# Kernel optimization log

Hardware: AMD Instinct MI355X
Metric: run time of the kernel (lower is better)

Reference implementation:

```python
import jax, jax.numpy as jnp
import numpy as np

DIM = 256
WS = 7          # window_size
NH = 8          # num_heads
HD = DIM // NH  # head_dim = 32
SCALE = HD ** (-0.5)
B = 4096        # batch * num_windows
N = WS * WS     # 49 tokens per window


def _rel_pos_index(ws):
    coords = np.stack(np.meshgrid(np.arange(ws), np.arange(ws), indexing='ij'))
    cf = coords.transpose(1, 2, 0).reshape(-1, 2)                 # [N,2]
    rel = cf[:, None, :] - cf[None, :, :]                          # [N,N,2]
    rel[:, :, 0] += ws - 1
    rel[:, :, 1] += ws - 1
    rel[:, :, 0] *= 2 * ws - 1
    return jnp.asarray(rel.sum(-1).astype(np.int32))               # [N,N]

REL_IDX = _rel_pos_index(WS)


def setup_inputs() -> dict:
    key = jax.random.key(0)
    ks = jax.random.split(key, 8)
    x = jax.random.normal(ks[0], (B, N, DIM), dtype=jnp.float32)
    mask = jax.random.normal(ks[1], (B, 1, N, N), dtype=jnp.float32)
    qkv_w = jax.random.normal(ks[2], (DIM, 3 * DIM), dtype=jnp.float32) * 0.02
    qkv_b = jnp.zeros((3 * DIM,), dtype=jnp.float32)
    rpb_table = jax.random.normal(ks[3], ((2 * WS - 1) ** 2, NH), dtype=jnp.float32) * 0.02
    proj_w = jax.random.normal(ks[4], (DIM, DIM), dtype=jnp.float32) * 0.02
    proj_b = jnp.zeros((DIM,), dtype=jnp.float32)
    return {"x": x, "mask": mask, "qkv_w": qkv_w, "qkv_b": qkv_b,
            "rpb_table": rpb_table, "proj_w": proj_w, "proj_b": proj_b}


def reference(x, mask, qkv_w, qkv_b, rpb_table, proj_w, proj_b):
    b, n, c = x.shape
    qkv = x @ qkv_w + qkv_b                                        # [b,n,3c]
    qkv = qkv.reshape(b, n, 3, NH, HD).transpose(2, 0, 3, 1, 4)    # [3,b,h,n,d]
    q, k, v = qkv[0], qkv[1], qkv[2]
    attn = jnp.einsum('bhnd,bhmd->bhnm', q * SCALE, k)             # [b,h,n,n]
    bias = rpb_table[REL_IDX.reshape(-1)].reshape(n, n, NH)        # [n,n,h]
    attn = attn + bias.transpose(2, 0, 1)[None] + mask             # [b,h,n,n]
    attn = jax.nn.softmax(attn, axis=-1)
    out = jnp.einsum('bhnm,bhmd->bhnd', attn, v)                   # [b,h,n,d]
    out = out.transpose(0, 2, 1, 3).reshape(b, n, c)               # [b,n,c]
    return out @ proj_w + proj_b
```

## Files before the change

### kernel.cpp

```cpp
#include <hip/hip_runtime.h>
#include <cstdint>
#include <cstddef>


#define NTOK 49
#define SCALE 0.17677669529663687f

typedef unsigned short u16;
typedef __attribute__((ext_vector_type(8))) short short8;
typedef __attribute__((ext_vector_type(4))) float f32x4;

__device__ __forceinline__ u16 f2bf(float f) {
    unsigned int u = __float_as_uint(f);
    u = (u + 0x7FFFu + ((u >> 16) & 1u)) >> 16;
    return (u16)u;
}

__device__ __forceinline__ void async_lds16(void* lds, const void* g) {
    __builtin_amdgcn_global_load_lds(
        (const __attribute__((address_space(1))) void*)g,
        (__attribute__((address_space(3))) void*)lds, 16, 0, 0);
}

__global__ void prep_weights(const float* __restrict__ qkv_w,
                             const float* __restrict__ proj_w,
                             u16* __restrict__ qkv_wT,
                             u16* __restrict__ proj_wT) {
    int i = blockIdx.x * 256 + threadIdx.x;
    if (i < 768 * 256) {
        int oc = i >> 8, k = i & 255;
        qkv_wT[i] = f2bf(qkv_w[k * 768 + oc]);
    }
    int j = i - 768 * 256;
    if (j >= 0 && j < 256 * 256) {
        int oc = j >> 8, k = j & 255;
        proj_wT[j] = f2bf(proj_w[k * 256 + oc]);
    }
}

__global__ __launch_bounds__(512, 4) void qkv_gemm(
        const float* __restrict__ x, const u16* __restrict__ wT,
        const float* __restrict__ bias, u16* __restrict__ qkv) {
    __shared__ __align__(16) u16 As[128 * 64];
    __shared__ __align__(16) u16 Bs[256 * 64];
    const int bid = blockIdx.x;
    const int m0 = (bid % 1568) * 128, n0 = (bid / 1568) * 256;
    const int t = threadIdx.x;
    const int lane = t & 63, w = t >> 6;
    const int quad = lane >> 4, l16 = lane & 15;
    const int wm = w & 1, wn = w >> 1;
    const int ar = t >> 2, ac = (t & 3) * 16;
    const int br = t >> 3, bc = (t & 7) * 8;
    f32x4 acc[4][4] = {};
    for (int kk = 0; kk < 256; kk += 64) {
        #pragma unroll
        for (int c = 0; c < 4; ++c)
            async_lds16(&Bs[c * 4096 + t * 8],
                        wT + (size_t)(n0 + c * 64 + br) * 256 + kk + bc);
        {
            const float* src = x + (size_t)(m0 + ar) * 256 + kk + ac;
            const f32x4 v0 = *(const f32x4*)(src);
            const f32x4 v1 = *(const f32x4*)(src + 4);
            const f32x4 v2 = *(const f32x4*)(src + 8);
            const f32x4 v3 = *(const f32x4*)(src + 12);
            ushort4 p0, p1, p2, p3;
            p0.x=f2bf(v0.x); p0.y=f2bf(v0.y); p0.z=f2bf(v0.z); p0.w=f2bf(v0.w);
            p1.x=f2bf(v1.x); p1.y=f2bf(v1.y); p1.z=f2bf(v1.z); p1.w=f2bf(v1.w);
            p2.x=f2bf(v2.x); p2.y=f2bf(v2.y); p2.z=f2bf(v2.z); p2.w=f2bf(v2.w);
            p3.x=f2bf(v3.x); p3.y=f2bf(v3.y); p3.z=f2bf(v3.z); p3.w=f2bf(v3.w);
            uint4 q0, q1;
            q0.x=*(unsigned*)&p0.x; q0.y=*(unsigned*)&p0.z;
            q0.z=*(unsigned*)&p1.x; q0.w=*(unsigned*)&p1.z;
            q1.x=*(unsigned*)&p2.x; q1.y=*(unsigned*)&p2.z;
            q1.z=*(unsigned*)&p3.x; q1.w=*(unsigned*)&p3.z;
            *(uint4*)&As[ar * 64 + ac] = q0;
            *(uint4*)&As[ar * 64 + ac + 8] = q1;
        }
        __syncthreads();
        #pragma unroll
        for (int ks = 0; ks < 2; ++ks) {
            short8 af[4], bfr[4];
            #pragma unroll
            for (int i = 0; i < 4; ++i)
                af[i] = *(const short8*)&As[(wm * 64 + i * 16 + l16) * 64 + ks * 32 + quad * 8];
            #pragma unroll
            for (int j = 0; j < 4; ++j)
                bfr[j] = *(const short8*)&Bs[(wn * 64 + j * 16 + l16) * 64 + ks * 32 + quad * 8];
            #pragma unroll
            for (int i = 0; i < 4; ++i)
                #pragma unroll
                for (int j = 0; j < 4; ++j)
                    acc[i][j] = __builtin_amdgcn_mfma_f32_16x16x32_bf16(
                        af[i], bfr[j], acc[i][j], 0, 0, 0);
        }
        __syncthreads();
    }
    #pragma unroll
    for (int j = 0; j < 4; ++j) {
        const int gc = n0 + wn * 64 + j * 16 + l16;
        const float bv = bias[gc];
        const float scl = (gc < 256) ? SCALE : 1.0f;
        #pragma unroll
        for (int i = 0; i < 4; ++i) {
            const int gr = m0 + wm * 64 + i * 16 + quad * 4;
            #pragma unroll
            for (int r = 0; r < 4; ++r)
                qkv[(size_t)(gr + r) * 768 + gc] = f2bf((acc[i][j][r] + bv) * scl);
        }
    }
}

__global__ __launch_bounds__(512, 4) void attn_proj(
        const u16* __restrict__ qkv, const float* __restrict__ mask,
        const float* __restrict__ rpb, const u16* __restrict__ projT,
        const float* __restrict__ proj_b, float* __restrict__ out) {
    __shared__ __align__(16) u16 Vt[8][32 * 68];
    __shared__ __align__(16) u16 OutS[49][264];
    const int b = blockIdx.x;
    const int t = threadIdx.x;
    const int lane = t & 63, h = t >> 6;
    const int quad = lane >> 4, l16 = lane & 15;
    const short8 zf = {0, 0, 0, 0, 0, 0, 0, 0};
    const f32x4 zero4 = {0.f, 0.f, 0.f, 0.f};

    {
        unsigned int* vz = (unsigned int*)&Vt[0][0];
        for (int i = t; i < 8 * 32 * 68 / 2; i += 512) vz[i] = 0;
    }
    __syncthreads();
    const u16* qrow = qkv + (size_t)b * NTOK * 768;
    for (int idx = t; idx < NTOK * 64; idx += 512) {
        const int n = idx >> 6, hd = (idx & 63) * 4;
        const ushort4 v = *(const ushort4*)(qrow + n * 768 + 512 + hd);
        u16* vt = &Vt[hd >> 5][0];
        const int d = hd & 31;
        vt[(d + 0) * 68 + n] = v.x;
        vt[(d + 1) * 68 + n] = v.y;
        vt[(d + 2) * 68 + n] = v.z;
        vt[(d + 3) * 68 + n] = v.w;
    }
    __syncthreads();

    short8 bK[4];
    #pragma unroll
    for (int j = 0; j < 4; ++j) {
        const int r = j * 16 + l16;
        bK[j] = (r < NTOK) ? *(const short8*)(qrow + r * 768 + 256 + h * 32 + quad * 8) : zf;
    }
    short8 bV[2][2];
    #pragma unroll
    for (int ct = 0; ct < 2; ++ct)
        #pragma unroll
        for (int ks = 0; ks < 2; ++ks)
            bV[ct][ks] = *(const short8*)&Vt[h][(ct * 16 + l16) * 68 + ks * 32 + quad * 8];
    __threadfence_block();

    u16* Ps = &Vt[h][0];
    const float* mrow = mask + (size_t)b * (NTOK * NTOK);
    int cc[4], c7[4], cm[4];
    #pragma unroll
    for (int j = 0; j < 4; ++j) {
        cc[j] = j * 16 + l16;
        c7[j] = (cc[j] * 37) >> 8;
        cm[j] = cc[j] - c7[j] * 7;
    }

    #pragma unroll
    for (int i = 0; i < 4; ++i) {
        const int qr = i * 16 + l16;
        const short8 aQ = (qr < NTOK)
            ? *(const short8*)(qrow + qr * 768 + h * 32 + quad * 8) : zf;
        f32x4 S[4];
        #pragma unroll
        for (int j = 0; j < 4; ++j)
            S[j] = __builtin_amdgcn_mfma_f32_16x16x32_bf16(aQ, bK[j], zero4, 0, 0, 0);
        #pragma unroll
        for (int r = 0; r < 4; ++r) {
            const int row = i * 16 + quad * 4 + r;
            const int r7 = (row * 37) >> 8;
            const int rm = row - r7 * 7;
            #pragma unroll
            for (int j = 0; j < 4; ++j) {
                float s = -1e30f;
                if (row < NTOK && cc[j] < NTOK) {
                    const int idx = (r7 - c7[j] + 6) * 13 + (rm - cm[j] + 6);
                    s = S[j][r] + rpb[idx * 8 + h] + mrow[row * 49 + cc[j]];
                }
                S[j][r] = s;
            }
            float mx = fmaxf(fmaxf(S[0][r], S[1][r]), fmaxf(S[2][r], S[3][r]));
            #pragma unroll
            for (int off = 1; off < 16; off <<= 1) mx = fmaxf(mx, __shfl_xor(mx, off));
            float sum = 0.f;
            #pragma unroll
            for (int j = 0; j < 4; ++j) {
                const float e = __expf(S[j][r] - mx);
                S[j][r] = e;
                sum += e;
            }
            #pragma unroll
            for (int off = 1; off < 16; off <<= 1) sum += __shfl_xor(sum, off);
            const float rinv = 1.0f / sum;
            #pragma unroll
            for (int j = 0; j < 4; ++j) S[j][r] = S[j][r] * rinv;
        }
        __threadfence_block();
        #pragma unroll
        for (int j = 0; j < 4; ++j)
            #pragma unroll
            for (int r = 0; r < 4; ++r)
                Ps[(quad * 4 + r) * 68 + j * 16 + l16] = f2bf(S[j][r]);
        __threadfence_block();
        const short8 aP0 = *(const short8*)&Ps[l16 * 68 + quad * 8];
        const short8 aP1 = *(const short8*)&Ps[l16 * 68 + 32 + quad * 8];
        f32x4 O0 = __builtin_amdgcn_mfma_f32_16x16x32_bf16(aP0, bV[0][0], zero4, 0, 0, 0);
        O0 = __builtin_amdgcn_mfma_f32_16x16x32_bf16(aP1, bV[0][1], O0, 0, 0, 0);
        f32x4 O1 = __builtin_amdgcn_mfma_f32_16x16x32_bf16(aP0, bV[1][0], zero4, 0, 0, 0);
        O1 = __builtin_amdgcn_mfma_f32_16x16x32_bf16(aP1, bV[1][1], O1, 0, 0, 0);
        #pragma unroll
        for (int r = 0; r < 4; ++r) {
            const int row = i * 16 + quad * 4 + r;
            if (row < NTOK) {
                OutS[row][h * 32 + l16] = f2bf(O0[r]);
                OutS[row][h * 32 + 16 + l16] = f2bf(O1[r]);
            }
        }
    }
    __syncthreads();

    f32x4 P2[4][2] = {};
    #pragma unroll
    for (int ks = 0; ks < 8; ++ks) {
        short8 bW[2];
        #pragma unroll
        for (int ct = 0; ct < 2; ++ct)
            bW[ct] = *(const short8*)(projT + (size_t)(h * 32 + ct * 16 + l16) * 256
                                      + ks * 32 + quad * 8);
        #pragma unroll
        for (int i = 0; i < 4; ++i) {
            const int row = i * 16 + l16;
            const short8 aO = (row < NTOK) ? *(const short8*)&OutS[row][ks * 32 + quad * 8] : zf;
            #pragma unroll
            for (int ct = 0; ct < 2; ++ct)
                P2[i][ct] = __builtin_amdgcn_mfma_f32_16x16x32_bf16(aO, bW[ct], P2[i][ct], 0, 0, 0);
        }
    }
    #pragma unroll
    for (int ct = 0; ct < 2; ++ct) {
        const int gc = h * 32 + ct * 16 + l16;
        const float pb = proj_b[gc];
        #pragma unroll
        for (int i = 0; i < 4; ++i)
            #pragma unroll
            for (int r = 0; r < 4; ++r) {
                const int row = i * 16 + quad * 4 + r;
                if (row < NTOK)
                    out[((size_t)b * NTOK + row) * 256 + gc] = P2[i][ct][r] + pb;
            }
    }
}

extern "C" void kernel_launch(void* const* d_in, const int* in_sizes, int n_in,
                              void* d_out, int out_size, void* d_ws, size_t ws_size,
                              hipStream_t stream) {
    const float* x      = (const float*)d_in[0];
    const float* mask   = (const float*)d_in[1];
    const float* qkv_w  = (const float*)d_in[2];
    const float* qkv_b  = (const float*)d_in[3];
    const float* rpb    = (const float*)d_in[4];
    const float* proj_w = (const float*)d_in[5];
    const float* proj_b = (const float*)d_in[6];
    float* outp = (float*)d_out;

    u16* qkv     = (u16*)d_ws;
    u16* qkv_wT  = qkv + (size_t)200704 * 768;
    u16* proj_wT = qkv_wT + 768 * 256;

    prep_weights<<<1024, 256, 0, stream>>>(qkv_w, proj_w, qkv_wT, proj_wT);
    qkv_gemm<<<1568 * 3, 512, 0, stream>>>(x, qkv_wT, qkv_b, qkv);
    attn_proj<<<4096, 512, 0, stream>>>(qkv, mask, rpb, proj_wT, proj_b, outp);
}
```

Before: 826.4 us.

## Precompute bias table, stage mask in LDS, transpose QK and shuffle P via bpermute

The relative-position bias is expanded once into a padded per-head 64x64 table in the prep kernel, so the gather with index arithmetic disappears from attention. The attention kernel stages each window's mask in LDS and computes S transposed (K as the A operand), which lets each lane hold a full query column and shortens the softmax reductions to two shuffles. Probabilities are packed with v_cvt_pk_bf16 and redistributed with ds_bpermute rather than a round trip through LDS. V is transposed per head with packed stores, LDS use shrinks so the launch bound can target 6 blocks per CU, and qkv_gemm block order is swizzled. Risks include register pressure at the higher occupancy target and the bpermute lane mapping being subtle.

```diff
diff --git a/kernel.cpp b/kernel.cpp
--- a/kernel.cpp
+++ b/kernel.cpp
@@ -16,6 +16,12 @@
     return (u16)u;
 }
 
+__device__ __forceinline__ unsigned cvt_pk_bf16(float lo, float hi) {
+    unsigned r;
+    asm("v_cvt_pk_bf16_f32 %0, %1, %2" : "=v"(r) : "v"(lo), "v"(hi));
+    return r;
+}
+
 __device__ __forceinline__ void async_lds16(void* lds, const void* g) {
     __builtin_amdgcn_global_load_lds(
         (const __attribute__((address_space(1))) void*)g,
@@ -24,8 +30,10 @@
 
 __global__ void prep_weights(const float* __restrict__ qkv_w,
                              const float* __restrict__ proj_w,
+                             const float* __restrict__ rpb,
                              u16* __restrict__ qkv_wT,
-                             u16* __restrict__ proj_wT) {
+                             u16* __restrict__ proj_wT,
+                             float* __restrict__ bias_p) {
     int i = blockIdx.x * 256 + threadIdx.x;
     if (i < 768 * 256) {
         int oc = i >> 8, k = i & 255;
@@ -35,6 +43,17 @@
     if (j >= 0 && j < 256 * 256) {
         int oc = j >> 8, k = j & 255;
         proj_wT[j] = f2bf(proj_w[k * 256 + oc]);
+    }
+    int m = i - (768 * 256 + 256 * 256);
+    if (m >= 0 && m < 8 * 64 * 64) {
+        int h = m >> 12, q = (m >> 6) & 63, k = m & 63;
+        float v = -1e30f;
+        if (q < NTOK && k < NTOK) {
+            int qr = q / 7, qc = q - qr * 7;
+            int kr = k / 7, kc = k - kr * 7;
+            v = rpb[((qr - kr + 6) * 13 + (qc - kc + 6)) * 8 + h];
+        }
+        bias_p[m] = v;
     }
 }
 
@@ -43,7 +62,8 @@
         const float* __restrict__ bias, u16* __restrict__ qkv) {
     __shared__ __align__(16) u16 As[128 * 64];
     __shared__ __align__(16) u16 Bs[256 * 64];
-    const int bid = blockIdx.x;
+    const int b0 = blockIdx.x;
+    const int bid = (b0 & 7) * 588 + (b0 >> 3);
     const int m0 = (bid % 1568) * 128, n0 = (bid / 1568) * 256;
     const int t = threadIdx.x;
     const int lane = t & 63, w = t >> 6;
@@ -110,119 +130,133 @@
     }
 }
 
-__global__ __launch_bounds__(512, 4) void attn_proj(
+__global__ __launch_bounds__(512, 6) void attn_proj(
         const u16* __restrict__ qkv, const float* __restrict__ mask,
-        const float* __restrict__ rpb, const u16* __restrict__ projT,
+        const float* __restrict__ bias_p, const u16* __restrict__ projT,
         const float* __restrict__ proj_b, float* __restrict__ out) {
-    __shared__ __align__(16) u16 Vt[8][32 * 68];
-    __shared__ __align__(16) u16 OutS[49][264];
+    __shared__ __align__(16) u16 SMEM[8 * 32 * 68];
+    __shared__ __align__(16) float maskL[49 * 68];
     const int b = blockIdx.x;
     const int t = threadIdx.x;
     const int lane = t & 63, h = t >> 6;
     const int quad = lane >> 4, l16 = lane & 15;
     const short8 zf = {0, 0, 0, 0, 0, 0, 0, 0};
     const f32x4 zero4 = {0.f, 0.f, 0.f, 0.f};
+    const u16* qrow = qkv + (size_t)b * NTOK * 768;
+    const float* mrow = mask + (size_t)b * (NTOK * NTOK);
 
     {
-        unsigned int* vz = (unsigned int*)&Vt[0][0];
-        for (int i = t; i < 8 * 32 * 68 / 2; i += 512) vz[i] = 0;
+        unsigned* vw = (unsigned*)&SMEM[h * 2176];
+        const int tp = lane & 31;
+        const int dh = (lane >> 5) * 4;
+        const int n0 = 2 * tp;
+        #pragma unroll
+        for (int it = 0; it < 4; ++it) {
+            const int d0 = it * 8 + dh;
+            ushort4 g0 = {0, 0, 0, 0}, g1 = {0, 0, 0, 0};
+            if (n0 < NTOK)     g0 = *(const ushort4*)(qrow + n0 * 768 + 512 + h * 32 + d0);
+            if (n0 + 1 < NTOK) g1 = *(const ushort4*)(qrow + (n0 + 1) * 768 + 512 + h * 32 + d0);
+            vw[(d0 + 0) * 34 + tp] = (unsigned)g0.x | ((unsigned)g1.x << 16);
+            vw[(d0 + 1) * 34 + tp] = (unsigned)g0.y | ((unsigned)g1.y << 16);
+            vw[(d0 + 2) * 34 + tp] = (unsigned)g0.z | ((unsigned)g1.z << 16);
+            vw[(d0 + 3) * 34 + tp] = (unsigned)g0.w | ((unsigned)g1.w << 16);
+        }
+    }
+    for (int r = h; r < NTOK; r += 8) {
+        maskL[r * 68 + lane] = (lane < NTOK) ? mrow[r * 49 + lane] : 0.f;
+        if (lane < 4) maskL[r * 68 + 64 + lane] = 0.f;
     }
     __syncthreads();
-    const u16* qrow = qkv + (size_t)b * NTOK * 768;
-    for (int idx = t; idx < NTOK * 64; idx += 512) {
-        const int n = idx >> 6, hd = (idx & 63) * 4;
-        const ushort4 v = *(const ushort4*)(qrow + n * 768 + 512 + hd);
-        u16* vt = &Vt[hd >> 5][0];
-        const int d = hd & 31;
-        vt[(d + 0) * 68 + n] = v.x;
-        vt[(d + 1) * 68 + n] = v.y;
-        vt[(d + 2) * 68 + n] = v.z;
-        vt[(d + 3) * 68 + n] = v.w;
+
+    short8 bV[2][2];
+    {
+        const u16* vt = &SMEM[h * 2176];
+        #pragma unroll
+        for (int ct = 0; ct < 2; ++ct)
+            #pragma unroll
+            for (int ks = 0; ks < 2; ++ks)
+                bV[ct][ks] = *(const short8*)&vt[(ct * 16 + l16) * 68 + ks * 32 + quad * 8];
+    }
+    short8 aK[4];
+    #pragma unroll
+    for (int ki = 0; ki < 4; ++ki) {
+        const int kt = ki * 16 + l16;
+        aK[ki] = (kt < NTOK) ? *(const short8*)(qrow + kt * 768 + 256 + h * 32 + quad * 8) : zf;
     }
     __syncthreads();
 
-    short8 bK[4];
-    #pragma unroll
-    for (int j = 0; j < 4; ++j) {
-        const int r = j * 16 + l16;
-        bK[j] = (r < NTOK) ? *(const short8*)(qrow + r * 768 + 256 + h * 32 + quad * 8) : zf;
-    }
-    short8 bV[2][2];
-    #pragma unroll
-    for (int ct = 0; ct < 2; ++ct)
-        #pragma unroll
-        for (int ks = 0; ks < 2; ++ks)
-            bV[ct][ks] = *(const short8*)&Vt[h][(ct * 16 + l16) * 68 + ks * 32 + quad * 8];
-    __threadfence_block();
-
-    u16* Ps = &Vt[h][0];
-    const float* mrow = mask + (size_t)b * (NTOK * NTOK);
-    int cc[4], c7[4], cm[4];
-    #pragma unroll
-    for (int j = 0; j < 4; ++j) {
-        cc[j] = j * 16 + l16;
-        c7[j] = (cc[j] * 37) >> 8;
-        cm[j] = cc[j] - c7[j] * 7;
-    }
-
-    #pragma unroll
-    for (int i = 0; i < 4; ++i) {
-        const int qr = i * 16 + l16;
-        const short8 aQ = (qr < NTOK)
-            ? *(const short8*)(qrow + qr * 768 + h * 32 + quad * 8) : zf;
+    u16* OutS = SMEM;
+    const float* bias_h = bias_p + (h << 12);
+    const int saA = (((quad & 1) << 5) + l16) << 2;
+    const int saB = saA + 64;
+    const bool hiK = (quad >> 1) != 0;
+
+    #pragma unroll
+    for (int qj = 0; qj < 4; ++qj) {
+        const int qtok = qj * 16 + l16;
+        const short8 bQ = (qtok < NTOK)
+            ? *(const short8*)(qrow + qtok * 768 + h * 32 + quad * 8) : zf;
         f32x4 S[4];
         #pragma unroll
-        for (int j = 0; j < 4; ++j)
-            S[j] = __builtin_amdgcn_mfma_f32_16x16x32_bf16(aQ, bK[j], zero4, 0, 0, 0);
-        #pragma unroll
-        for (int r = 0; r < 4; ++r) {
-            const int row = i * 16 + quad * 4 + r;
-            const int r7 = (row * 37) >> 8;
-            const int rm = row - r7 * 7;
-            #pragma unroll
-            for (int j = 0; j < 4; ++j) {
-                float s = -1e30f;
-                if (row < NTOK && cc[j] < NTOK) {
-                    const int idx = (r7 - c7[j] + 6) * 13 + (rm - cm[j] + 6);
-                    s = S[j][r] + rpb[idx * 8 + h] + mrow[row * 49 + cc[j]];
-                }
-                S[j][r] = s;
-            }
-            float mx = fmaxf(fmaxf(S[0][r], S[1][r]), fmaxf(S[2][r], S[3][r]));
-            #pragma unroll
-            for (int off = 1; off < 16; off <<= 1) mx = fmaxf(mx, __shfl_xor(mx, off));
-            float sum = 0.f;
-            #pragma unroll
-            for (int j = 0; j < 4; ++j) {
-                const float e = __expf(S[j][r] - mx);
-                S[j][r] = e;
+        for (int ki = 0; ki < 4; ++ki)
+            S[ki] = __builtin_amdgcn_mfma_f32_16x16x32_bf16(aK[ki], bQ, zero4, 0, 0, 0);
+        const int qc = (qtok < NTOK) ? qtok : 0;
+        #pragma unroll
+        for (int ki = 0; ki < 4; ++ki) {
+            const f32x4 bb = *(const f32x4*)(bias_h + qtok * 64 + ki * 16 + quad * 4);
+            const f32x4 mm = *(const f32x4*)(&maskL[qc * 68 + ki * 16 + quad * 4]);
+            S[ki] += bb + mm;
+        }
+        float mx = fmaxf(fmaxf(fmaxf(S[0][0], S[0][1]), fmaxf(S[0][2], S[0][3])),
+                         fmaxf(fmaxf(S[1][0], S[1][1]), fmaxf(S[1][2], S[1][3])));
+        mx = fmaxf(mx, fmaxf(fmaxf(fmaxf(S[2][0], S[2][1]), fmaxf(S[2][2], S[2][3])),
+                             fmaxf(fmaxf(S[3][0], S[3][1]), fmaxf(S[3][2], S[3][3]))));
+        mx = fmaxf(mx, __shfl_xor(mx, 16));
+        mx = fmaxf(mx, __shfl_xor(mx, 32));
+        float sum = 0.f;
+        #pragma unroll
+        for (int ki = 0; ki < 4; ++ki)
+            #pragma unroll
+            for (int r = 0; r < 4; ++r) {
+                const float e = __expf(S[ki][r] - mx);
+                S[ki][r] = e;
                 sum += e;
             }
-            #pragma unroll
-            for (int off = 1; off < 16; off <<= 1) sum += __shfl_xor(sum, off);
-            const float rinv = 1.0f / sum;
-            #pragma unroll
-            for (int j = 0; j < 4; ++j) S[j][r] = S[j][r] * rinv;
-        }
-        __threadfence_block();
-        #pragma unroll
-        for (int j = 0; j < 4; ++j)
-            #pragma unroll
-            for (int r = 0; r < 4; ++r)
-                Ps[(quad * 4 + r) * 68 + j * 16 + l16] = f2bf(S[j][r]);
-        __threadfence_block();
-        const short8 aP0 = *(const short8*)&Ps[l16 * 68 + quad * 8];
-        const short8 aP1 = *(const short8*)&Ps[l16 * 68 + 32 + quad * 8];
-        f32x4 O0 = __builtin_amdgcn_mfma_f32_16x16x32_bf16(aP0, bV[0][0], zero4, 0, 0, 0);
-        O0 = __builtin_amdgcn_mfma_f32_16x16x32_bf16(aP1, bV[0][1], O0, 0, 0, 0);
-        f32x4 O1 = __builtin_amdgcn_mfma_f32_16x16x32_bf16(aP0, bV[1][0], zero4, 0, 0, 0);
-        O1 = __builtin_amdgcn_mfma_f32_16x16x32_bf16(aP1, bV[1][1], O1, 0, 0, 0);
+        sum += __shfl_xor(sum, 16);
+        sum += __shfl_xor(sum, 32);
+        const float rinv = 1.0f / sum;
+        unsigned pk2[4][2];
+        #pragma unroll
+        for (int ki = 0; ki < 4; ++ki) {
+            pk2[ki][0] = cvt_pk_bf16(S[ki][0] * rinv, S[ki][1] * rinv);
+            pk2[ki][1] = cvt_pk_bf16(S[ki][2] * rinv, S[ki][3] * rinv);
+        }
+        f32x4 O0 = zero4, O1 = zero4;
+        #pragma unroll
+        for (int ks = 0; ks < 2; ++ks) {
+            const int j0 = 2 * ks, j1 = 2 * ks + 1;
+            const unsigned a0 = __builtin_amdgcn_ds_bpermute(saA, (int)pk2[j0][0]);
+            const unsigned b0 = __builtin_amdgcn_ds_bpermute(saA, (int)pk2[j1][0]);
+            const unsigned a1 = __builtin_amdgcn_ds_bpermute(saA, (int)pk2[j0][1]);
+            const unsigned b1 = __builtin_amdgcn_ds_bpermute(saA, (int)pk2[j1][1]);
+            const unsigned a2 = __builtin_amdgcn_ds_bpermute(saB, (int)pk2[j0][0]);
+            const unsigned b2 = __builtin_amdgcn_ds_bpermute(saB, (int)pk2[j1][0]);
+            const unsigned a3 = __builtin_amdgcn_ds_bpermute(saB, (int)pk2[j0][1]);
+            const unsigned b3 = __builtin_amdgcn_ds_bpermute(saB, (int)pk2[j1][1]);
+            union { unsigned u[4]; short8 s; } ap;
+            ap.u[0] = hiK ? b0 : a0;
+            ap.u[1] = hiK ? b1 : a1;
+            ap.u[2] = hiK ? b2 : a2;
+            ap.u[3] = hiK ? b3 : a3;
+            O0 = __builtin_amdgcn_mfma_f32_16x16x32_bf16(ap.s, bV[0][ks], O0, 0, 0, 0);
+            O1 = __builtin_amdgcn_mfma_f32_16x16x32_bf16(ap.s, bV[1][ks], O1, 0, 0, 0);
+        }
         #pragma unroll
         for (int r = 0; r < 4; ++r) {
-            const int row = i * 16 + quad * 4 + r;
+            const int row = qj * 16 + quad * 4 + r;
             if (row < NTOK) {
-                OutS[row][h * 32 + l16] = f2bf(O0[r]);
-                OutS[row][h * 32 + 16 + l16] = f2bf(O1[r]);
+                OutS[row * 264 + h * 32 + l16]      = f2bf(O0[r]);
+                OutS[row * 264 + h * 32 + 16 + l16] = f2bf(O1[r]);
             }
         }
     }
@@ -239,7 +273,7 @@
         #pragma unroll
         for (int i = 0; i < 4; ++i) {
             const int row = i * 16 + l16;
-            const short8 aO = (row < NTOK) ? *(const short8*)&OutS[row][ks * 32 + quad * 8] : zf;
+            const short8 aO = (row < NTOK) ? *(const short8*)&OutS[row * 264 + ks * 32 + quad * 8] : zf;
             #pragma unroll
             for (int ct = 0; ct < 2; ++ct)
                 P2[i][ct] = __builtin_amdgcn_mfma_f32_16x16x32_bf16(aO, bW[ct], P2[i][ct], 0, 0, 0);
@@ -272,11 +306,12 @@
     const float* proj_b = (const float*)d_in[6];
     float* outp = (float*)d_out;
 
-    u16* qkv     = (u16*)d_ws;
-    u16* qkv_wT  = qkv + (size_t)200704 * 768;
-    u16* proj_wT = qkv_wT + 768 * 256;
-
-    prep_weights<<<1024, 256, 0, stream>>>(qkv_w, proj_w, qkv_wT, proj_wT);
+    u16* qkv      = (u16*)d_ws;
+    u16* qkv_wT   = qkv + (size_t)200704 * 768;
+    u16* proj_wT  = qkv_wT + 768 * 256;
+    float* bias_p = (float*)(proj_wT + 256 * 256);
+
+    prep_weights<<<1152, 256, 0, stream>>>(qkv_w, proj_w, rpb, qkv_wT, proj_wT, bias_p);
     qkv_gemm<<<1568 * 3, 512, 0, stream>>>(x, qkv_wT, qkv_b, qkv);
-    attn_proj<<<4096, 512, 0, stream>>>(qkv, mask, rpb, proj_wT, proj_b, outp);
-}
+    attn_proj<<<4096, 512, 0, stream>>>(qkv, mask, bias_p, proj_wT, proj_b, outp);
+}
```

New measurement: 897.1 us. 8.6% more time.
